# Kernel optimization log

Hardware: AMD Instinct MI355X
Metric: run time of the kernel (lower is better)

## Reference

```python
import jax, jax.numpy as jnp
import numpy as np

B, S, D, H, F = 4, 2048, 1024, 16, 4096
BS = 64               # sparse attention block size
DH = D // H           # head dim
EPS = 1e-5


def _layer_norm(x, g, b):
    m = jnp.mean(x, axis=-1, keepdims=True)
    v = jnp.mean(jnp.square(x - m), axis=-1, keepdims=True)
    return (x - m) * jax.lax.rsqrt(v + EPS) * g + b


def setup_inputs() -> dict:
    key = jax.random.key(0)
    ks = jax.random.split(key, 12)
    sc = 0.02
    return {
        "hidden_states": jax.random.normal(ks[0], (B, S, D), dtype=jnp.float32),
        "ln1_g": jnp.ones((D,), jnp.float32), "ln1_b": jnp.zeros((D,), jnp.float32),
        "ln2_g": jnp.ones((D,), jnp.float32), "ln2_b": jnp.zeros((D,), jnp.float32),
        "wq": jax.random.normal(ks[1], (D, D), jnp.float32) * sc, "bq": jnp.zeros((D,), jnp.float32),
        "wk": jax.random.normal(ks[2], (D, D), jnp.float32) * sc, "bk": jnp.zeros((D,), jnp.float32),
        "wv": jax.random.normal(ks[3], (D, D), jnp.float32) * sc, "bv": jnp.zeros((D,), jnp.float32),
        "wo": jax.random.normal(ks[4], (D, D), jnp.float32) * sc, "bo": jnp.zeros((D,), jnp.float32),
        "w1": jax.random.normal(ks[5], (D, F), jnp.float32) * sc, "b1": jnp.zeros((F,), jnp.float32),
        "w2": jax.random.normal(ks[6], (F, D), jnp.float32) * sc, "b2": jnp.zeros((D,), jnp.float32),
    }


def _heads(x, w, b):
    # [B,S,D] -> [B,H,S/BS,BS,DH] block layout
    y = (x @ w + b).reshape(B, S, H, DH).transpose(0, 2, 1, 3)
    return y.reshape(B, H, S // BS, BS, DH)


def _block_attention(x, wq, bq, wk, bk, wv, bv, wo, bo):
    q = _heads(x, wq, bq)
    k = _heads(x, wk, bk)
    v = _heads(x, wv, bv)
    scores = jnp.einsum("bhnqd,bhnkd->bhnqk", q, k) / jnp.sqrt(jnp.float32(DH))
    w = jax.nn.softmax(scores, axis=-1)           # block-local (sparse) attention weights
    o = jnp.einsum("bhnqk,bhnkd->bhnqd", w, v)
    o = o.reshape(B, H, S, DH).transpose(0, 2, 1, 3).reshape(B, S, D)
    return o @ wo + bo, w


def reference(hidden_states, ln1_g, ln1_b, ln2_g, ln2_b,
              wq, bq, wk, bk, wv, bv, wo, bo, w1, b1, w2, b2):
    # pre-norm attention + residual
    x1 = _layer_norm(hidden_states, ln1_g, ln1_b)
    attn_out, attn_w = _block_attention(x1, wq, bq, wk, bk, wv, bv, wo, bo)
    h = hidden_states + attn_out
    # pre-norm FFN + residual (exact GELU, matching torch nn.GELU default)
    x2 = _layer_norm(h, ln2_g, ln2_b)
    ff = jax.nn.gelu(x2 @ w1 + b1, approximate=False) @ w2 + b2
    return h + ff, attn_w
```

## Files before the change

### kernel.cpp

```cpp
#include <hip/hip_runtime.h>
#include <hip/hip_bf16.h>
#include <cmath>

using bf16 = __hip_bfloat16;
typedef __attribute__((ext_vector_type(8))) short short8;
typedef __attribute__((ext_vector_type(4))) float f32x4;

#define LDK 72

__device__ __forceinline__ float bf2f(bf16 v){ return __bfloat162float(v); }
__device__ __forceinline__ bf16 f2bf(float v){ return __float2bfloat16(v); }

__device__ __forceinline__ void ld16(const void* g, void* l) {
    __builtin_amdgcn_global_load_lds(
        (const __attribute__((address_space(1))) void*)g,
        (__attribute__((address_space(3))) void*)l, 16, 0, 0);
}

__device__ __forceinline__ float gelu_f(float x) {
    float u = 0.7978845608028654f * x * (1.0f + 0.044715f * x * x);
    float e = __expf(2.0f * u);
    float t = 1.0f - 2.0f / (e + 1.0f);
    return 0.5f * x * (1.0f + t);
}

__global__ __launch_bounds__(256) void transpose_f32_bf16(
    const float* __restrict__ in, bf16* __restrict__ out, int R, int C)
{
    __shared__ __align__(16) bf16 tile[64][72];
    const int c0 = blockIdx.x * 64, r0 = blockIdx.y * 64;
    const int t = threadIdx.x;
    const int lr = t >> 3, lc = (t & 7) * 8;
    for (int p = 0; p < 2; ++p) {
        int r = p * 32 + lr;
        const float* src = in + (size_t)(r0 + r) * C + c0 + lc;
        float4 a = *(const float4*)src;
        float4 b = *(const float4*)(src + 4);
        tile[r][lc + 0] = f2bf(a.x); tile[r][lc + 1] = f2bf(a.y);
        tile[r][lc + 2] = f2bf(a.z); tile[r][lc + 3] = f2bf(a.w);
        tile[r][lc + 4] = f2bf(b.x); tile[r][lc + 5] = f2bf(b.y);
        tile[r][lc + 6] = f2bf(b.z); tile[r][lc + 7] = f2bf(b.w);
    }
    __syncthreads();
    for (int p = 0; p < 2; ++p) {
        int r = p * 32 + lr;
        short8 v;
        for (int j = 0; j < 8; ++j) v[j] = *(const short*)&tile[lc + j][r];
        *(short8*)(out + (size_t)(c0 + r) * R + r0 + lc) = v;
    }
}

__global__ __launch_bounds__(256) void concat_bias(
    const float* __restrict__ bq, const float* __restrict__ bk,
    const float* __restrict__ bv, float* __restrict__ out)
{
    int i = blockIdx.x * 256 + threadIdx.x;
    const float* src = (i < 1024) ? bq : ((i < 2048) ? bk : bv);
    out[i] = src[i & 1023];
}

__global__ __launch_bounds__(256) void layernorm_k(
    const float* __restrict__ x, const float* __restrict__ g,
    const float* __restrict__ bta, bf16* __restrict__ out)
{
    const int row = blockIdx.x, t = threadIdx.x;
    const float* xr = x + (size_t)row * 1024;
    float v[4], s1 = 0.f, s2 = 0.f;
    for (int j = 0; j < 4; ++j) {
        float f = xr[j * 256 + t];
        v[j] = f; s1 += f; s2 += f * f;
    }
    for (int d = 1; d < 64; d <<= 1) { s1 += __shfl_xor(s1, d); s2 += __shfl_xor(s2, d); }
    __shared__ float red[2][4];
    int wave = t >> 6, lane = t & 63;
    if (lane == 0) { red[0][wave] = s1; red[1][wave] = s2; }
    __syncthreads();
    s1 = red[0][0] + red[0][1] + red[0][2] + red[0][3];
    s2 = red[1][0] + red[1][1] + red[1][2] + red[1][3];
    float mean = s1 * (1.0f / 1024.0f);
    float var  = s2 * (1.0f / 1024.0f) - mean * mean;
    float rs   = rsqrtf(var + 1e-5f);
    bf16* orow = out + (size_t)row * 1024;
    for (int j = 0; j < 4; ++j) {
        int c = j * 256 + t;
        orow[c] = f2bf((v[j] - mean) * rs * g[c] + bta[c]);
    }
}

template <int MODE>
__global__ __launch_bounds__(512, 2) void gemm256(
    const bf16* __restrict__ A, const bf16* __restrict__ Bt,
    const float* __restrict__ bias, void* __restrict__ C,
    int M, int N, int K)
{
    __shared__ __align__(16) bf16 smem[2][2][256 * 32];
    const int m0 = blockIdx.x * 256, n0 = blockIdx.y * 256;
    const int t = threadIdx.x;
    const int wave = t >> 6, lane = t & 63, lhi = lane >> 4, llo = lane & 15;
    const int wm = (wave >> 2) * 128;
    const int wn = (wave & 3) * 64;

    const int r_st = wave * 16 + (lane >> 2);
    const int gsw  = (lane & 3) ^ ((r_st >> 1) & 3);
    const bf16* Abase = A  + (size_t)(m0 + r_st) * K + gsw * 8;
    const bf16* Bbase = Bt + (size_t)(n0 + r_st) * K + gsw * 8;

    auto stageA = [&](int j, int b) {
        const bf16* s = Abase + j * 32;
        ld16(s,                   &smem[b][0][wave * 512]);
        ld16(s + (size_t)128 * K, &smem[b][0][(8 + wave) * 512]);
    };
    auto stageB = [&](int j, int b) {
        const bf16* s = Bbase + j * 32;
        ld16(s,                   &smem[b][1][wave * 512]);
        ld16(s + (size_t)128 * K, &smem[b][1][(8 + wave) * 512]);
    };
    const int grd = (llo >> 1) & 3;
    auto rdA = [&](int b, int mi) {
        return *(const short8*)&smem[b][0][(wm + mi * 16 + llo) * 32 + ((lhi ^ grd) * 8)];
    };
    auto rdB = [&](int b, int ni) {
        return *(const short8*)&smem[b][1][(wn + ni * 16 + llo) * 32 + ((lhi ^ grd) * 8)];
    };

    f32x4 acc[8][4];
    #pragma unroll
    for (int i = 0; i < 8; ++i)
        #pragma unroll
        for (int j = 0; j < 4; ++j) acc[i][j] = (f32x4){0.f, 0.f, 0.f, 0.f};

    const int T = K >> 5;
    stageA(0, 0); stageB(0, 0);

    for (int j = 0; j < T; ++j) {
        const int cb = j & 1;
        if (j + 1 < T) {
            stageA(j + 1, cb ^ 1);
            stageB(j + 1, cb ^ 1);
            asm volatile("s_waitcnt vmcnt(4)" ::: "memory");
        } else {
            asm volatile("s_waitcnt vmcnt(0)" ::: "memory");
        }
        __builtin_amdgcn_sched_barrier(0);
        __builtin_amdgcn_s_barrier();
        __builtin_amdgcn_sched_barrier(0);

        short8 af[8], bfr[4];
        #pragma unroll
        for (int mi = 0; mi < 8; ++mi) af[mi] = rdA(cb, mi);
        #pragma unroll
        for (int ni = 0; ni < 4; ++ni) bfr[ni] = rdB(cb, ni);
        __builtin_amdgcn_s_setprio(1);
        #pragma unroll
        for (int mi = 0; mi < 8; ++mi)
            #pragma unroll
            for (int ni = 0; ni < 4; ++ni)
                acc[mi][ni] = __builtin_amdgcn_mfma_f32_16x16x32_bf16(
                    af[mi], bfr[ni], acc[mi][ni], 0, 0, 0);
        __builtin_amdgcn_s_setprio(0);

        if (j + 1 < T) {
            asm volatile("s_waitcnt lgkmcnt(0)" ::: "memory");
            __builtin_amdgcn_sched_barrier(0);
            __builtin_amdgcn_s_barrier();
            __builtin_amdgcn_sched_barrier(0);
        }
    }

    #pragma unroll
    for (int mi = 0; mi < 8; ++mi)
        #pragma unroll
        for (int ni = 0; ni < 4; ++ni) {
            int row = m0 + wm + mi * 16 + lhi * 4;
            int col = n0 + wn + ni * 16 + llo;
            float bcol = bias[col];
            #pragma unroll
            for (int r = 0; r < 4; ++r) {
                size_t idx = (size_t)(row + r) * N + col;
                float v = acc[mi][ni][r] + bcol;
                if (MODE == 2) ((bf16*)C)[idx] = f2bf(gelu_f(v));
                else           ((bf16*)C)[idx] = f2bf(v);
            }
        }
}

template <int MODE, int TM>
__global__ __launch_bounds__(256) void gemm_bt(
    const bf16* __restrict__ A, const bf16* __restrict__ Bt,
    const float* __restrict__ bias, const float* __restrict__ res,
    void* __restrict__ C, int M, int N, int K)
{
    constexpr int MI = TM / 32;
    __shared__ __align__(16) bf16 As[TM * 64];
    __shared__ __align__(16) bf16 Bs[128 * 64];
    const int m0 = blockIdx.x * TM, n0 = blockIdx.y * 128;
    const int t = threadIdx.x;
    const int wave = t >> 6, lane = t & 63, lhi = lane >> 4, llo = lane & 15;
    const int wm = (wave & 1) * (TM / 2), wn = (wave >> 1) * 64;
    const int lrow = lane >> 3;
    const int lcolsw = ((lane & 7) ^ lrow) * 8;

    const bf16* Ag = A  + (size_t)(m0 + lrow) * K + lcolsw;
    const bf16* Bg = Bt + (size_t)(n0 + lrow) * K + lcolsw;

    f32x4 acc[MI][4];
    for (int i = 0; i < MI; ++i)
        for (int j = 0; j < 4; ++j) acc[i][j] = (f32x4){0.f, 0.f, 0.f, 0.f};

    auto issue = [&](int k0) {
        for (int p = 0; p < TM / 32; ++p) {
            int rb = wave * (TM / 4) + p * 8;
            ld16(Ag + (size_t)rb * K + k0, &As[rb * 64]);
        }
        for (int p = 0; p < 4; ++p) {
            int rb = wave * 32 + p * 8;
            ld16(Bg + (size_t)rb * K + k0, &Bs[rb * 64]);
        }
    };
    auto compute = [&]() {
        for (int kk = 0; kk < 64; kk += 32) {
            const int gb = kk >> 3;
            short8 af[MI], bfr[4];
            for (int i = 0; i < MI; ++i) {
                int row = wm + i * 16 + llo;
                af[i] = *(const short8*)&As[row * 64 + (((gb + lhi) ^ (llo & 7)) * 8)];
            }
            for (int i = 0; i < 4; ++i) {
                int row = wn + i * 16 + llo;
                bfr[i] = *(const short8*)&Bs[row * 64 + (((gb + lhi) ^ (llo & 7)) * 8)];
            }
            for (int mi = 0; mi < MI; ++mi)
                for (int ni = 0; ni < 4; ++ni)
                    acc[mi][ni] = __builtin_amdgcn_mfma_f32_16x16x32_bf16(
                        af[mi], bfr[ni], acc[mi][ni], 0, 0, 0);
        }
    };

    issue(0);
    __syncthreads();
    for (int k0 = 0; ; ) {
        compute();
        k0 += 64;
        if (k0 >= K) break;
        __syncthreads();
        issue(k0);
        __syncthreads();
    }

    for (int mi = 0; mi < MI; ++mi)
        for (int ni = 0; ni < 4; ++ni) {
            int row = m0 + wm + mi * 16 + lhi * 4;
            int col = n0 + wn + ni * 16 + llo;
            float bcol = bias[col];
            for (int r = 0; r < 4; ++r) {
                size_t idx = (size_t)(row + r) * N + col;
                float v = acc[mi][ni][r] + bcol;
                if (MODE == 0) {
                    ((bf16*)C)[idx] = f2bf(v);
                } else if (MODE == 1) {
                    ((float*)C)[idx] = v + res[idx];
                } else if (MODE == 2) {
                    ((bf16*)C)[idx] = f2bf(gelu_f(v));
                } else {
                    ((float*)C)[idx] = v + res[idx];
                }
            }
        }
}

__global__ __launch_bounds__(256) void attn_kernel(
    const bf16* __restrict__ qkv, float* __restrict__ attw, bf16* __restrict__ o)
{
    __shared__ __align__(16) bf16 qs[64][LDK];
    __shared__ __align__(16) bf16 ks[64][LDK];
    __shared__ __align__(16) bf16 vs[64][LDK];
    const int gid = blockIdx.x;
    const int blk = gid & 31, h = (gid >> 5) & 15, b = gid >> 9;
    const int t = threadIdx.x, wave = t >> 6, lane = t & 63;
    const int lhi = lane >> 4, llo = lane & 15;
    const int srow = t >> 3, scol = (t & 7) * 8;

    for (int p = 0; p < 2; ++p) {
        int r = p * 32 + srow;
        const bf16* base = qkv + (size_t)(b * 2048 + blk * 64 + r) * 3072 + h * 64 + scol;
        *(short8*)&qs[r][scol] = *(const short8*)(base);
        *(short8*)&ks[r][scol] = *(const short8*)(base + 1024);
        *(short8*)&vs[r][scol] = *(const short8*)(base + 2048);
    }
    __syncthreads();

    f32x4 sacc[4];
    for (int j = 0; j < 4; ++j) sacc[j] = (f32x4){0.f, 0.f, 0.f, 0.f};
    for (int kk = 0; kk < 64; kk += 32) {
        short8 aq = *(const short8*)&qs[wave * 16 + llo][kk + lhi * 8];
        for (int j = 0; j < 4; ++j) {
            short8 bk = *(const short8*)&ks[j * 16 + llo][kk + lhi * 8];
            sacc[j] = __builtin_amdgcn_mfma_f32_16x16x32_bf16(aq, bk, sacc[j], 0, 0, 0);
        }
    }
    float inv[4];
    for (int r = 0; r < 4; ++r) {
        float m = -1e30f;
        for (int j = 0; j < 4; ++j) m = fmaxf(m, sacc[j][r]);
        for (int d = 1; d < 16; d <<= 1) m = fmaxf(m, __shfl_xor(m, d));
        float s = 0.f;
        for (int j = 0; j < 4; ++j) {
            float e = expf((sacc[j][r] - m) * 0.125f);
            sacc[j][r] = e; s += e;
        }
        for (int d = 1; d < 16; d <<= 1) s += __shfl_xor(s, d);
        inv[r] = 1.0f / s;
    }
    __syncthreads();
    const size_t wbase = (size_t)gid * 4096;
    for (int j = 0; j < 4; ++j)
        for (int r = 0; r < 4; ++r) {
            int row = wave * 16 + lhi * 4 + r, col = j * 16 + llo;
            float pw = sacc[j][r] * inv[r];
            qs[row][col] = f2bf(pw);
            attw[wbase + row * 64 + col] = pw;
        }
    __syncthreads();

    f32x4 oacc[4];
    for (int nt = 0; nt < 4; ++nt) oacc[nt] = (f32x4){0.f, 0.f, 0.f, 0.f};
    for (int kk = 0; kk < 64; kk += 32) {
        short8 aw = *(const short8*)&qs[wave * 16 + llo][kk + lhi * 8];
        for (int nt = 0; nt < 4; ++nt) {
            short8 bv;
            for (int jj = 0; jj < 8; ++jj)
                bv[jj] = *(const short*)&vs[kk + lhi * 8 + jj][nt * 16 + llo];
            oacc[nt] = __builtin_amdgcn_mfma_f32_16x16x32_bf16(aw, bv, oacc[nt], 0, 0, 0);
        }
    }
    for (int nt = 0; nt < 4; ++nt)
        for (int r = 0; r < 4; ++r) {
            int row = wave * 16 + lhi * 4 + r, col = nt * 16 + llo;
            o[(size_t)(b * 2048 + blk * 64 + row) * 1024 + h * 64 + col] = f2bf(oacc[nt][r]);
        }
}

extern "C" void kernel_launch(void* const* d_in, const int* in_sizes, int n_in,
                              void* d_out, int out_size, void* d_ws, size_t ws_size,
                              hipStream_t stream)
{
    const float* hidden = (const float*)d_in[0];
    const float* ln1_g  = (const float*)d_in[1];
    const float* ln1_b  = (const float*)d_in[2];
    const float* ln2_g  = (const float*)d_in[3];
    const float* ln2_b  = (const float*)d_in[4];
    const float* wq = (const float*)d_in[5];  const float* bq = (const float*)d_in[6];
    const float* wk = (const float*)d_in[7];  const float* bk = (const float*)d_in[8];
    const float* wv = (const float*)d_in[9];  const float* bv = (const float*)d_in[10];
    const float* wo = (const float*)d_in[11]; const float* bo = (const float*)d_in[12];
    const float* w1 = (const float*)d_in[13]; const float* b1 = (const float*)d_in[14];
    const float* w2 = (const float*)d_in[15]; const float* b2 = (const float*)d_in[16];

    char* ws = (char*)d_ws;
    const size_t MB = 1u << 20;
    bf16*  wqkvT   = (bf16*)(ws +  0 * MB);
    bf16*  woT     = (bf16*)(ws +  6 * MB);
    bf16*  w1T     = (bf16*)(ws +  8 * MB);
    bf16*  w2T     = (bf16*)(ws + 16 * MB);
    float* biasQKV = (float*)(ws + 24 * MB);
    bf16*  x       = (bf16*)(ws + 25 * MB);
    bf16*  qkv     = (bf16*)(ws + 41 * MB);
    float* hbuf    = (float*)(ws + 41 * MB);
    bf16*  ffc     = (bf16*)(ws + 73 * MB);
    bf16*  obuf    = (bf16*)(ws + 89 * MB);

    float* out0 = (float*)d_out;
    float* attw = (float*)d_out + (size_t)8192 * 1024;

    transpose_f32_bf16<<<dim3(16, 16), 256, 0, stream>>>(wq, wqkvT,                 1024, 1024);
    transpose_f32_bf16<<<dim3(16, 16), 256, 0, stream>>>(wk, wqkvT + 1024 * 1024,   1024, 1024);
    transpose_f32_bf16<<<dim3(16, 16), 256, 0, stream>>>(wv, wqkvT + 2*1024*1024,   1024, 1024);
    transpose_f32_bf16<<<dim3(16, 16), 256, 0, stream>>>(wo, woT, 1024, 1024);
    transpose_f32_bf16<<<dim3(64, 16), 256, 0, stream>>>(w1, w1T, 1024, 4096);
    transpose_f32_bf16<<<dim3(16, 64), 256, 0, stream>>>(w2, w2T, 4096, 1024);
    concat_bias<<<12, 256, 0, stream>>>(bq, bk, bv, biasQKV);

    layernorm_k<<<8192, 256, 0, stream>>>(hidden, ln1_g, ln1_b, x);

    gemm256<0><<<dim3(32, 12), 512, 0, stream>>>(x, wqkvT, biasQKV, qkv,
                                                 8192, 3072, 1024);

    attn_kernel<<<2048, 256, 0, stream>>>(qkv, attw, obuf);

    gemm_bt<1, 128><<<dim3(64, 8), 256, 0, stream>>>(obuf, woT, bo, hidden, hbuf,
                                                     8192, 1024, 1024);

    layernorm_k<<<8192, 256, 0, stream>>>(hbuf, ln2_g, ln2_b, x);

    gemm256<2><<<dim3(32, 16), 512, 0, stream>>>(x, w1T, b1, ffc,
                                                 8192, 4096, 1024);

    gemm_bt<3, 128><<<dim3(64, 8), 256, 0, stream>>>(ffc, w2T, b2, hbuf, out0,
                                                     8192, 1024, 4096);
}
```

Baseline: 449.1 us.

## Restructure 256x256 GEMM with K=64 tiles and quadrant-interleaved staging

```diff
diff --git a/kernel.cpp b/kernel.cpp
--- a/kernel.cpp
+++ b/kernel.cpp
@@ -87,40 +87,45 @@
     }
 }
 
-template <int MODE>
-__global__ __launch_bounds__(512, 2) void gemm256(
+template <int MODE, int KT>
+__global__ __launch_bounds__(512, 1) void gemm256(
     const bf16* __restrict__ A, const bf16* __restrict__ Bt,
     const float* __restrict__ bias, void* __restrict__ C,
-    int M, int N, int K)
-{
-    __shared__ __align__(16) bf16 smem[2][2][256 * 32];
+    int M, int N)
+{
+    __shared__ __align__(16) bf16 smem[2][2][256 * 64];
     const int m0 = blockIdx.x * 256, n0 = blockIdx.y * 256;
     const int t = threadIdx.x;
     const int wave = t >> 6, lane = t & 63, lhi = lane >> 4, llo = lane & 15;
     const int wm = (wave >> 2) * 128;
     const int wn = (wave & 3) * 64;
-
-    const int r_st = wave * 16 + (lane >> 2);
-    const int gsw  = (lane & 3) ^ ((r_st >> 1) & 3);
-    const bf16* Abase = A  + (size_t)(m0 + r_st) * K + gsw * 8;
-    const bf16* Bbase = Bt + (size_t)(n0 + r_st) * K + gsw * 8;
-
-    auto stageA = [&](int j, int b) {
-        const bf16* s = Abase + j * 32;
-        ld16(s,                   &smem[b][0][wave * 512]);
-        ld16(s + (size_t)128 * K, &smem[b][0][(8 + wave) * 512]);
-    };
-    auto stageB = [&](int j, int b) {
-        const bf16* s = Bbase + j * 32;
-        ld16(s,                   &smem[b][1][wave * 512]);
-        ld16(s + (size_t)128 * K, &smem[b][1][(8 + wave) * 512]);
-    };
-    const int grd = (llo >> 1) & 3;
-    auto rdA = [&](int b, int mi) {
-        return *(const short8*)&smem[b][0][(wm + mi * 16 + llo) * 32 + ((lhi ^ grd) * 8)];
-    };
-    auto rdB = [&](int b, int ni) {
-        return *(const short8*)&smem[b][1][(wn + ni * 16 + llo) * 32 + ((lhi ^ grd) * 8)];
+    const int lrow = lane >> 3, lcol = lane & 7;
+    const int gsrc = (lcol ^ lrow) * 8;
+
+    const bf16* Ag = A  + (size_t)(m0 + lrow) * KT + gsrc;
+    const bf16* Bg = Bt + (size_t)(n0 + lrow) * KT + gsrc;
+
+    const int axb = (wave >> 2) * 128 + (wave & 3) * 8;
+    const int bxb = (wave & 3) * 64 + (wave >> 2) * 16;
+
+    auto stgA = [&](int kt, int b, int yoff) {
+        const bf16* s = Ag + (size_t)(axb + yoff) * KT + kt * 64;
+        ld16(s,                  &smem[b][0][(axb + yoff) * 64]);
+        ld16(s + (size_t)32 * KT, &smem[b][0][(axb + yoff + 32) * 64]);
+    };
+    auto stgB = [&](int kt, int b, int yoff) {
+        const bf16* s = Bg + (size_t)(bxb + yoff) * KT + kt * 64;
+        ld16(s,                  &smem[b][1][(bxb + yoff) * 64]);
+        ld16(s + (size_t)8 * KT, &smem[b][1][(bxb + yoff + 8) * 64]);
+    };
+    const int swz = llo & 7;
+    auto rdA = [&](int b, int mi, int kk) {
+        int R = wm + mi * 16 + llo;
+        return *(const short8*)&smem[b][0][R * 64 + (((kk * 4 + lhi) ^ swz) * 8)];
+    };
+    auto rdB = [&](int b, int ni, int kk) {
+        int R = wn + ni * 16 + llo;
+        return *(const short8*)&smem[b][1][R * 64 + (((kk * 4 + lhi) ^ swz) * 8)];
     };
 
     f32x4 acc[8][4];
@@ -129,43 +134,132 @@
         #pragma unroll
         for (int j = 0; j < 4; ++j) acc[i][j] = (f32x4){0.f, 0.f, 0.f, 0.f};
 
-    const int T = K >> 5;
-    stageA(0, 0); stageB(0, 0);
-
-    for (int j = 0; j < T; ++j) {
-        const int cb = j & 1;
-        if (j + 1 < T) {
-            stageA(j + 1, cb ^ 1);
-            stageB(j + 1, cb ^ 1);
-            asm volatile("s_waitcnt vmcnt(4)" ::: "memory");
-        } else {
-            asm volatile("s_waitcnt vmcnt(0)" ::: "memory");
-        }
-        __builtin_amdgcn_sched_barrier(0);
-        __builtin_amdgcn_s_barrier();
-        __builtin_amdgcn_sched_barrier(0);
-
-        short8 af[8], bfr[4];
-        #pragma unroll
-        for (int mi = 0; mi < 8; ++mi) af[mi] = rdA(cb, mi);
-        #pragma unroll
-        for (int ni = 0; ni < 4; ++ni) bfr[ni] = rdB(cb, ni);
-        __builtin_amdgcn_s_setprio(1);
-        #pragma unroll
-        for (int mi = 0; mi < 8; ++mi)
-            #pragma unroll
-            for (int ni = 0; ni < 4; ++ni)
-                acc[mi][ni] = __builtin_amdgcn_mfma_f32_16x16x32_bf16(
-                    af[mi], bfr[ni], acc[mi][ni], 0, 0, 0);
-        __builtin_amdgcn_s_setprio(0);
-
-        if (j + 1 < T) {
-            asm volatile("s_waitcnt lgkmcnt(0)" ::: "memory");
-            __builtin_amdgcn_sched_barrier(0);
-            __builtin_amdgcn_s_barrier();
-            __builtin_amdgcn_sched_barrier(0);
-        }
-    }
+    constexpr int T = KT / 64;
+    stgA(0, 0, 0); stgB(0, 0, 0); stgA(0, 0, 64); stgB(0, 0, 32);
+
+#define SB __builtin_amdgcn_sched_barrier(0)
+
+    #pragma unroll 2
+    for (int j = 0; j < T - 1; ++j) {
+        const int cb = j & 1, nb = cb ^ 1;
+        short8 aX[4][2], bX[2][2], aY[4][2], bY[2][2];
+        stgA(j + 1, nb, 0);
+        asm volatile("s_waitcnt vmcnt(6)" ::: "memory");
+        SB; __builtin_amdgcn_s_barrier(); SB;
+        #pragma unroll
+        for (int mi = 0; mi < 4; ++mi)
+            #pragma unroll
+            for (int kk = 0; kk < 2; ++kk) aX[mi][kk] = rdA(cb, mi, kk);
+        #pragma unroll
+        for (int ni = 0; ni < 2; ++ni)
+            #pragma unroll
+            for (int kk = 0; kk < 2; ++kk) bX[ni][kk] = rdB(cb, ni, kk);
+        __builtin_amdgcn_s_setprio(1);
+        #pragma unroll
+        for (int mi = 0; mi < 4; ++mi)
+            #pragma unroll
+            for (int ni = 0; ni < 2; ++ni)
+                #pragma unroll
+                for (int kk = 0; kk < 2; ++kk)
+                    acc[mi][ni] = __builtin_amdgcn_mfma_f32_16x16x32_bf16(
+                        aX[mi][kk], bX[ni][kk], acc[mi][ni], 0, 0, 0);
+        __builtin_amdgcn_s_setprio(0);
+        stgB(j + 1, nb, 0);
+        asm volatile("s_waitcnt vmcnt(4)" ::: "memory");
+        SB; __builtin_amdgcn_s_barrier(); SB;
+        #pragma unroll
+        for (int ni = 0; ni < 2; ++ni)
+            #pragma unroll
+            for (int kk = 0; kk < 2; ++kk) bY[ni][kk] = rdB(cb, ni + 2, kk);
+        __builtin_amdgcn_s_setprio(1);
+        #pragma unroll
+        for (int mi = 0; mi < 4; ++mi)
+            #pragma unroll
+            for (int ni = 0; ni < 2; ++ni)
+                #pragma unroll
+                for (int kk = 0; kk < 2; ++kk)
+                    acc[mi][ni + 2] = __builtin_amdgcn_mfma_f32_16x16x32_bf16(
+                        aX[mi][kk], bY[ni][kk], acc[mi][ni + 2], 0, 0, 0);
+        __builtin_amdgcn_s_setprio(0);
+        stgA(j + 1, nb, 64);
+        SB; __builtin_amdgcn_s_barrier(); SB;
+        #pragma unroll
+        for (int mi = 0; mi < 4; ++mi)
+            #pragma unroll
+            for (int kk = 0; kk < 2; ++kk) aY[mi][kk] = rdA(cb, mi + 4, kk);
+        __builtin_amdgcn_s_setprio(1);
+        #pragma unroll
+        for (int mi = 0; mi < 4; ++mi)
+            #pragma unroll
+            for (int ni = 0; ni < 2; ++ni)
+                #pragma unroll
+                for (int kk = 0; kk < 2; ++kk)
+                    acc[mi + 4][ni] = __builtin_amdgcn_mfma_f32_16x16x32_bf16(
+                        aY[mi][kk], bX[ni][kk], acc[mi + 4][ni], 0, 0, 0);
+        __builtin_amdgcn_s_setprio(0);
+        stgB(j + 1, nb, 32);
+        SB; __builtin_amdgcn_s_barrier(); SB;
+        __builtin_amdgcn_s_setprio(1);
+        #pragma unroll
+        for (int mi = 0; mi < 4; ++mi)
+            #pragma unroll
+            for (int ni = 0; ni < 2; ++ni)
+                #pragma unroll
+                for (int kk = 0; kk < 2; ++kk)
+                    acc[mi + 4][ni + 2] = __builtin_amdgcn_mfma_f32_16x16x32_bf16(
+                        aY[mi][kk], bY[ni][kk], acc[mi + 4][ni + 2], 0, 0, 0);
+        __builtin_amdgcn_s_setprio(0);
+    }
+    {
+        const int cb = (T - 1) & 1;
+        short8 aX[4][2], bX[2][2], aY[4][2], bY[2][2];
+        asm volatile("s_waitcnt vmcnt(4)" ::: "memory");
+        SB; __builtin_amdgcn_s_barrier(); SB;
+        #pragma unroll
+        for (int mi = 0; mi < 4; ++mi)
+            #pragma unroll
+            for (int kk = 0; kk < 2; ++kk) aX[mi][kk] = rdA(cb, mi, kk);
+        #pragma unroll
+        for (int ni = 0; ni < 2; ++ni)
+            #pragma unroll
+            for (int kk = 0; kk < 2; ++kk) bX[ni][kk] = rdB(cb, ni, kk);
+        __builtin_amdgcn_s_setprio(1);
+        #pragma unroll
+        for (int mi = 0; mi < 4; ++mi)
+            #pragma unroll
+            for (int ni = 0; ni < 2; ++ni)
+                #pragma unroll
+                for (int kk = 0; kk < 2; ++kk)
+                    acc[mi][ni] = __builtin_amdgcn_mfma_f32_16x16x32_bf16(
+                        aX[mi][kk], bX[ni][kk], acc[mi][ni], 0, 0, 0);
+        __builtin_amdgcn_s_setprio(0);
+        asm volatile("s_waitcnt vmcnt(0)" ::: "memory");
+        SB; __builtin_amdgcn_s_barrier(); SB;
+        #pragma unroll
+        for (int ni = 0; ni < 2; ++ni)
+            #pragma unroll
+            for (int kk = 0; kk < 2; ++kk) bY[ni][kk] = rdB(cb, ni + 2, kk);
+        #pragma unroll
+        for (int mi = 0; mi < 4; ++mi)
+            #pragma unroll
+            for (int kk = 0; kk < 2; ++kk) aY[mi][kk] = rdA(cb, mi + 4, kk);
+        __builtin_amdgcn_s_setprio(1);
+        #pragma unroll
+        for (int mi = 0; mi < 4; ++mi)
+            #pragma unroll
+            for (int ni = 0; ni < 2; ++ni)
+                #pragma unroll
+                for (int kk = 0; kk < 2; ++kk) {
+                    acc[mi][ni + 2] = __builtin_amdgcn_mfma_f32_16x16x32_bf16(
+                        aX[mi][kk], bY[ni][kk], acc[mi][ni + 2], 0, 0, 0);
+                    acc[mi + 4][ni] = __builtin_amdgcn_mfma_f32_16x16x32_bf16(
+                        aY[mi][kk], bX[ni][kk], acc[mi + 4][ni], 0, 0, 0);
+                    acc[mi + 4][ni + 2] = __builtin_amdgcn_mfma_f32_16x16x32_bf16(
+                        aY[mi][kk], bY[ni][kk], acc[mi + 4][ni + 2], 0, 0, 0);
+                }
+        __builtin_amdgcn_s_setprio(0);
+    }
+#undef SB
 
     #pragma unroll
     for (int mi = 0; mi < 8; ++mi)
@@ -382,8 +476,8 @@
 
     layernorm_k<<<8192, 256, 0, stream>>>(hidden, ln1_g, ln1_b, x);
 
-    gemm256<0><<<dim3(32, 12), 512, 0, stream>>>(x, wqkvT, biasQKV, qkv,
-                                                 8192, 3072, 1024);
+    gemm256<0, 1024><<<dim3(32, 12), 512, 0, stream>>>(x, wqkvT, biasQKV, qkv,
+                                                       8192, 3072);
 
     attn_kernel<<<2048, 256, 0, stream>>>(qkv, attw, obuf);
 
@@ -392,8 +486,8 @@
 
     layernorm_k<<<8192, 256, 0, stream>>>(hbuf, ln2_g, ln2_b, x);
 
-    gemm256<2><<<dim3(32, 16), 512, 0, stream>>>(x, w1T, b1, ffc,
-                                                 8192, 4096, 1024);
+    gemm256<2, 1024><<<dim3(32, 16), 512, 0, stream>>>(x, w1T, b1, ffc,
+                                                       8192, 4096);
 
     gemm_bt<3, 128><<<dim3(64, 8), 256, 0, stream>>>(ffc, w2T, b2, hbuf, out0,
                                                      8192, 1024, 4096);
```

After: 428.0 us. 4.7% less time.
